# Optimization experiments

Measured on AMD Instinct MI355X. Metric: run time of the kernel, lower is better.

Reference implementation:

```python
import jax, jax.numpy as jnp
import numpy as np

WIN = (7, 7)
SHIFT = (3, 3)
HEADS = 12


def _rel_index():
    wh, ww = WIN
    coords = np.stack(np.meshgrid(np.arange(wh), np.arange(ww), indexing='ij')).reshape(2, -1)
    rel = (coords[:, :, None] - coords[:, None, :]).transpose(1, 2, 0).astype(np.int64)
    rel[:, :, 0] += wh - 1
    rel[:, :, 1] += ww - 1
    rel[:, :, 0] *= 2 * ww - 1
    return rel.sum(-1).reshape(-1)  # [N*N]


def _attn_mask(pH, pW, sh, sw):
    wh, ww = WIN
    mask = np.zeros((pH, pW), np.float32)
    h_sl = [(0, pH - wh), (pH - wh, pH - sh), (pH - sh, pH)]
    w_sl = [(0, pW - ww), (pW - ww, pW - sw), (pW - sw, pW)]
    cnt = 0
    for hs in h_sl:
        for ws in w_sl:
            mask[hs[0]:hs[1], ws[0]:ws[1]] = cnt
            cnt += 1
    nw = (pH // wh) * (pW // ww)
    mask = mask.reshape(pH // wh, wh, pW // ww, ww).transpose(0, 2, 1, 3).reshape(nw, wh * ww)
    diff = mask[:, None, :] - mask[:, :, None]
    return jnp.asarray(np.where(diff != 0, -100.0, 0.0).astype(np.float32))  # [nw, N, N]


def setup_inputs() -> dict:
    key = jax.random.key(0)
    ks = jax.random.split(key, 6)
    C = 384
    return {
        'x': jax.random.normal(ks[0], (16, 56, 56, C), jnp.float32),
        'qkv_weight': jax.random.normal(ks[1], (3 * C, C), jnp.float32) * 0.02,
        'qkv_bias': jax.random.normal(ks[2], (3 * C,), jnp.float32) * 0.02,
        'proj_weight': jax.random.normal(ks[3], (C, C), jnp.float32) * 0.02,
        'proj_bias': jax.random.normal(ks[4], (C,), jnp.float32) * 0.02,
        'rel_table': jax.random.normal(ks[5], (169, HEADS), jnp.float32) * 0.02,
    }


def reference(x, qkv_weight, qkv_bias, proj_weight, proj_bias, rel_table):
    B, H, W, C = x.shape
    wh, ww = WIN
    pad_b = (wh - H % wh) % wh
    pad_r = (ww - W % ww) % ww
    xp = jnp.pad(x, ((0, 0), (0, pad_b), (0, pad_r), (0, 0)))
    pH, pW = H + pad_b, W + pad_r
    sh = 0 if wh >= pH else SHIFT[0]
    sw = 0 if ww >= pW else SHIFT[1]
    shifted = (sh + sw) > 0
    if shifted:
        xp = jnp.roll(xp, (-sh, -sw), axis=(1, 2))
    nwh, nww = pH // wh, pW // ww
    nw, N = nwh * nww, wh * ww
    # window partition -> [B*nw, N, C]
    xw = xp.reshape(B, nwh, wh, nww, ww, C).transpose(0, 1, 3, 2, 4, 5).reshape(B * nw, N, C)
    qkv = xw @ qkv_weight.T + qkv_bias
    qkv = qkv.reshape(B * nw, N, 3, HEADS, C // HEADS).transpose(2, 0, 3, 1, 4)
    q, k, v = qkv[0], qkv[1], qkv[2]  # [B*nw, heads, N, hd]
    q = q * (C // HEADS) ** -0.5
    attn = jnp.einsum('whnd,whmd->whnm', q, k)
    bias = rel_table[jnp.asarray(_rel_index())].reshape(N, N, HEADS).transpose(2, 0, 1)
    attn = attn + bias[None]
    if shifted:
        mask = _attn_mask(pH, pW, sh, sw)  # [nw, N, N]
        attn = (attn.reshape(B, nw, HEADS, N, N) + mask[None, :, None]).reshape(B * nw, HEADS, N, N)
    attn = jax.nn.softmax(attn, axis=-1)
    out = jnp.einsum('whnm,whmd->whnd', attn, v).transpose(0, 2, 1, 3).reshape(B * nw, N, C)
    out = out @ proj_weight.T + proj_bias
    out = out.reshape(B, nwh, nww, wh, ww, C).transpose(0, 1, 3, 2, 4, 5).reshape(B, pH, pW, C)
    if shifted:
        out = jnp.roll(out, (sh, sw), axis=(1, 2))
    return out[:, :H, :W, :]
```

## Files before the change

kernel.cpp:

```cpp
#include <hip/hip_runtime.h>

#define CCH 384
#define NHEADS 12
#define HDIM 32
#define NTOK 49
#define NWIN 1024
#define MROWS 50176
#define PSTR 72

typedef __attribute__((ext_vector_type(8))) short bf16x8;
typedef __attribute__((ext_vector_type(4))) float f32x4;

#define WAITVM_BAR(N) asm volatile("s_waitcnt vmcnt(" #N ")\n\ts_barrier" ::: "memory")
#define BAR() asm volatile("s_barrier" ::: "memory")

__device__ __forceinline__ unsigned short f2bf(float f) {
    unsigned u = __builtin_bit_cast(unsigned, f);
    u += 0x7FFFu + ((u >> 16) & 1u);
    return (unsigned short)(u >> 16);
}

__device__ __forceinline__ void g2lds16(const unsigned short* g, unsigned short* l) {
    __builtin_amdgcn_global_load_lds(
        (const __attribute__((address_space(1))) unsigned int*)g,
        (__attribute__((address_space(3))) unsigned int*)l,
        16, 0, 0);
}

__global__ void prep_kernel(const float* __restrict__ qkvw, const float* __restrict__ projw,
                            const float* __restrict__ rel_table,
                            unsigned short* __restrict__ wq, unsigned short* __restrict__ wp,
                            float* __restrict__ btt2) {
    int i = blockIdx.x * 256 + threadIdx.x;
    if (i < 3 * CCH * CCH) wq[i] = f2bf(qkvw[i]);
    if (i < CCH * CCH) wp[i] = f2bf(projw[i]);
    if (i < 4 * NHEADS * 16 * 64) {
        int cls = i / (NHEADS * 16 * 64);
        int rem = i - cls * (NHEADS * 16 * 64);
        int h = rem / (16 * 64);
        int rem2 = rem - h * (16 * 64);
        int rb = rem2 >> 6, cj = rem2 & 63;
        int jreg = 0;
        if (cj < NTOK) {
            int jy = cj / 7, jx = cj - jy * 7;
            int ry = (cls & 2) ? ((jy < 4) ? 1 : 2) : 0;
            int rx = (cls & 1) ? ((jx < 4) ? 1 : 2) : 0;
            jreg = ry * 3 + rx;
        }
        float4 o;
        float* po = (float*)&o;
#pragma unroll
        for (int rr = 0; rr < 4; ++rr) {
            int ri = rb * 4 + rr;
            float v = -1e30f;
            if (ri < NTOK && cj < NTOK) {
                int iy = ri / 7, ix = ri - iy * 7;
                int jy = cj / 7, jx = cj - jy * 7;
                int idx = (iy - jy + 6) * 13 + (ix - jx + 6);
                v = rel_table[idx * NHEADS + h];
                int ry = (cls & 2) ? ((iy < 4) ? 1 : 2) : 0;
                int rx = (cls & 1) ? ((ix < 4) ? 1 : 2) : 0;
                if (ry * 3 + rx != jreg) v -= 100.f;
            }
            po[rr] = v;
        }
        *(float4*)&btt2[(size_t)i * 4] = o;
    }
}

__device__ __forceinline__ size_t row_to_pixel(int r) {
    int wlin = r / 49, n = r - wlin * 49;
    int b = wlin >> 6, wimg = wlin & 63;
    int wy = wimg >> 3, wx = wimg & 7;
    int iy = n / 7, ix = n - iy * 7;
    int y = wy * 7 + iy + 3; if (y >= 56) y -= 56;
    int x = wx * 7 + ix + 3; if (x >= 56) x -= 56;
    return (size_t)((b * 56 + y) * 56 + x);
}

__global__ __launch_bounds__(256) void gather_kernel(const float* __restrict__ xin,
                                                     unsigned short* __restrict__ xw) {
    int idx = blockIdx.x * 256 + threadIdx.x;
    int row = idx / 96, c4 = (idx - row * 96) * 4;
    const float4 v = *(const float4*)(xin + row_to_pixel(row) * CCH + c4);
    ushort4 o;
    o.x = f2bf(v.x); o.y = f2bf(v.y); o.z = f2bf(v.z); o.w = f2bf(v.w);
    *(ushort4*)(xw + (size_t)row * CCH + c4) = o;
}

__global__ __launch_bounds__(512) void qkv_gemm(const unsigned short* __restrict__ xw,
        const unsigned short* __restrict__ wq, const float* __restrict__ qkv_bias,
        unsigned short* __restrict__ qb, unsigned short* __restrict__ kb,
        unsigned short* __restrict__ vb) {
    __shared__ unsigned short As[2][256 * 32];
    __shared__ unsigned short Bs[2][128 * 32];
    const int tid = threadIdx.x;
    const int bid = blockIdx.x;
    const int xcd = bid & 7;
    const int base = (xcd < 4) ? xcd * 221 : (4 * 221 + (xcd - 4) * 220);
    const int swz = base + (bid >> 3);
    const int rb = swz / 9, cb = swz - rb * 9;
    const int row0 = rb * 256;
    const int col0 = cb * 128;
    const int lane = tid & 63, wv = tid >> 6;
    const int wm = wv >> 1, wn = wv & 1;
    const int l15 = lane & 15, g = lane >> 4;

    const int lrow = lane >> 2;
    const int lc = lane & 3;
    const int scs = ((lc ^ ((lrow >> 1) & 3)) * 8);
    const unsigned short* gA0 = xw + (size_t)(row0 + wv * 32 + lrow) * CCH + scs;
    const unsigned short* gA1 = gA0 + (size_t)16 * CCH;
    const unsigned short* gB0 = wq + (size_t)(col0 + wv * 16 + lrow) * CCH + scs;
    const int rc = (g ^ ((l15 >> 1) & 3)) * 8;

    f32x4 acc[4][4];
#pragma unroll
    for (int i = 0; i < 4; ++i)
#pragma unroll
        for (int j = 0; j < 4; ++j) acc[i][j] = (f32x4){0.f, 0.f, 0.f, 0.f};

    g2lds16(gA0, &As[0][wv * 1024]);
    g2lds16(gA1, &As[0][wv * 1024 + 512]);
    g2lds16(gB0, &Bs[0][wv * 512]);

#pragma unroll
    for (int kk = 0; kk < 12; ++kk) {
        const int cur = kk & 1;
        if (kk < 11) {
            const int nxt = cur ^ 1;
            g2lds16(gA0 + (kk + 1) * 32, &As[nxt][wv * 1024]);
            g2lds16(gA1 + (kk + 1) * 32, &As[nxt][wv * 1024 + 512]);
            g2lds16(gB0 + (kk + 1) * 32, &Bs[nxt][wv * 512]);
            WAITVM_BAR(3);
        } else {
            WAITVM_BAR(0);
        }
        bf16x8 af[4], bfv[4];
#pragma unroll
        for (int mt = 0; mt < 4; ++mt)
            af[mt] = *(const bf16x8*)&As[cur][(wm * 64 + mt * 16 + l15) * 32 + rc];
#pragma unroll
        for (int nt = 0; nt < 4; ++nt)
            bfv[nt] = *(const bf16x8*)&Bs[cur][(wn * 64 + nt * 16 + l15) * 32 + rc];
#pragma unroll
        for (int mt = 0; mt < 4; ++mt)
#pragma unroll
            for (int nt = 0; nt < 4; ++nt)
                acc[mt][nt] = __builtin_amdgcn_mfma_f32_16x16x32_bf16(af[mt], bfv[nt], acc[mt][nt], 0, 0, 0);
        BAR();
    }

    const float SCALE = 0.17677669529663687f;
#pragma unroll
    for (int nt = 0; nt < 4; ++nt) {
        int col = col0 + wn * 64 + nt * 16 + l15;
        float bias = qkv_bias[col];
        int which = col / CCH;
        int rem = col - which * CCH;
        int h = rem >> 5, d = rem & 31;
        unsigned short* dstb = (which == 0) ? qb : ((which == 1) ? kb : vb);
        float scl = (which == 0) ? SCALE : 1.0f;
#pragma unroll
        for (int mt = 0; mt < 4; ++mt) {
#pragma unroll
            for (int rr = 0; rr < 4; ++rr) {
                int row = row0 + wm * 64 + mt * 16 + g * 4 + rr;
                int w2 = row / 49, n2 = row - w2 * 49;
                size_t inst = (size_t)(w2 * NHEADS + h);
                float v = (acc[mt][nt][rr] + bias) * scl;
                dstb[(inst * NTOK + n2) * HDIM + d] = f2bf(v);
            }
        }
    }
}

__global__ __launch_bounds__(256) void attn_kernel(const unsigned short* __restrict__ qbuf,
        const unsigned short* __restrict__ kbuf, const unsigned short* __restrict__ vbuf,
        const float* __restrict__ btt2, unsigned short* __restrict__ ao) {
    __shared__ unsigned short Ps[4][64 * PSTR];
    __shared__ unsigned short Vt[4][32 * 64];
    const int tid = threadIdx.x;
    const int lane = tid & 63, wv = tid >> 6;
    const int inst = blockIdx.x * 4 + wv;
    const int w = inst / NHEADS, h = inst - w * NHEADS;
    const int l15 = lane & 15, g = lane >> 4;
    const unsigned short* qp = qbuf + (size_t)inst * (NTOK * HDIM);
    const unsigned short* kp = kbuf + (size_t)inst * (NTOK * HDIM);
    const unsigned short* vp = vbuf + (size_t)inst * (NTOK * HDIM);

    const bf16x8 zero8 = {0, 0, 0, 0, 0, 0, 0, 0};
    bf16x8 vpre[4];
#pragma unroll
    for (int p = 0; p < 4; ++p) {
        int e0 = (p * 64 + lane) * 8;
        int tok = e0 >> 5;
        vpre[p] = (tok < NTOK) ? *(const bf16x8*)&vp[e0] : zero8;
    }

    bf16x8 aq[4], bk[4];
#pragma unroll
    for (int mt = 0; mt < 4; ++mt) {
        int row = mt * 16 + l15;
        aq[mt] = (row < NTOK) ? *(const bf16x8*)&qp[row * HDIM + g * 8] : zero8;
    }
#pragma unroll
    for (int nt = 0; nt < 4; ++nt) {
        int colk = nt * 16 + l15;
        bk[nt] = (colk < NTOK) ? *(const bf16x8*)&kp[colk * HDIM + g * 8] : zero8;
    }
    f32x4 s[4][4];
#pragma unroll
    for (int mt = 0; mt < 4; ++mt)
#pragma unroll
        for (int nt = 0; nt < 4; ++nt)
            s[mt][nt] = __builtin_amdgcn_mfma_f32_16x16x32_bf16(aq[mt], bk[nt], (f32x4){0.f, 0.f, 0.f, 0.f}, 0, 0, 0);

    {
        unsigned short* vt = Vt[wv];
#pragma unroll
        for (int p = 0; p < 4; ++p) {
            int e0 = (p * 64 + lane) * 8;
            int tok = e0 >> 5, d0 = e0 & 31;
#pragma unroll
            for (int j = 0; j < 8; ++j) {
                int d = d0 + j;
                vt[d * 64 + (tok ^ ((d & 7) << 3))] = (unsigned short)vpre[p][j];
            }
        }
    }

    const int wimg = w & 63;
    const int wy = wimg >> 3, wx = wimg & 7;
    const int wcls = (((wy == 7) ? 2 : 0) | ((wx == 7) ? 1 : 0));
    const float4* bt4 = (const float4*)btt2 + ((size_t)(wcls * NHEADS + h)) * (16 * 64);

    float inv[4][4];
#pragma unroll
    for (int mt = 0; mt < 4; ++mt) {
        float4 bias4[4];
#pragma unroll
        for (int nt = 0; nt < 4; ++nt)
            bias4[nt] = bt4[(mt * 4 + g) * 64 + nt * 16 + l15];
#pragma unroll
        for (int rr = 0; rr < 4; ++rr) {
#pragma unroll
            for (int nt = 0; nt < 4; ++nt) {
                float bb = (rr == 0) ? bias4[nt].x : (rr == 1) ? bias4[nt].y : (rr == 2) ? bias4[nt].z : bias4[nt].w;
                s[mt][nt][rr] += bb;
            }
            float m = fmaxf(fmaxf(s[mt][0][rr], s[mt][1][rr]), fmaxf(s[mt][2][rr], s[mt][3][rr]));
            m = fmaxf(m, __shfl_xor(m, 1));
            m = fmaxf(m, __shfl_xor(m, 2));
            m = fmaxf(m, __shfl_xor(m, 4));
            m = fmaxf(m, __shfl_xor(m, 8));
            float sum = 0.f;
#pragma unroll
            for (int nt = 0; nt < 4; ++nt) {
                float p = __expf(s[mt][nt][rr] - m);
                s[mt][nt][rr] = p;
                sum += p;
            }
            sum += __shfl_xor(sum, 1);
            sum += __shfl_xor(sum, 2);
            sum += __shfl_xor(sum, 4);
            sum += __shfl_xor(sum, 8);
            inv[mt][rr] = 1.0f / sum;
        }
    }
    unsigned short* ps = Ps[wv];
#pragma unroll
    for (int mt = 0; mt < 4; ++mt)
#pragma unroll
        for (int nt = 0; nt < 4; ++nt)
#pragma unroll
            for (int rr = 0; rr < 4; ++rr)
                ps[(mt * 16 + g * 4 + rr) * PSTR + nt * 16 + l15] = f2bf(s[mt][nt][rr]);

    f32x4 o[4][2];
#pragma unroll
    for (int mt = 0; mt < 4; ++mt)
#pragma unroll
        for (int dt = 0; dt < 2; ++dt) o[mt][dt] = (f32x4){0.f, 0.f, 0.f, 0.f};

    const unsigned short* vt = Vt[wv];
#pragma unroll
    for (int kt = 0; kt < 2; ++kt) {
        bf16x8 ap[4];
#pragma unroll
        for (int mt = 0; mt < 4; ++mt)
            ap[mt] = *(const bf16x8*)&ps[(mt * 16 + l15) * PSTR + kt * 32 + g * 8];
#pragma unroll
        for (int dt = 0; dt < 2; ++dt) {
            const int d = dt * 16 + l15;
            const int cb = kt * 32 + g * 8;
            bf16x8 bv = *(const bf16x8*)&vt[d * 64 + (cb ^ ((d & 7) << 3))];
#pragma unroll
            for (int mt = 0; mt < 4; ++mt)
                o[mt][dt] = __builtin_amdgcn_mfma_f32_16x16x32_bf16(ap[mt], bv, o[mt][dt], 0, 0, 0);
        }
    }
#pragma unroll
    for (int mt = 0; mt < 4; ++mt)
#pragma unroll
        for (int dt = 0; dt < 2; ++dt)
#pragma unroll
            for (int rr = 0; rr < 4; ++rr) {
                int row = mt * 16 + g * 4 + rr;
                if (row < NTOK) {
                    float val = o[mt][dt][rr] * inv[mt][rr];
                    ao[((size_t)(w * NTOK + row)) * CCH + h * HDIM + dt * 16 + l15] = f2bf(val);
                }
            }
}

__global__ __launch_bounds__(256) void proj_gemm(const unsigned short* __restrict__ ain,
        const unsigned short* __restrict__ wp, const float* __restrict__ proj_bias,
        float* __restrict__ out) {
    __shared__ unsigned short As[2][128 * 32];
    __shared__ unsigned short Bs[2][128 * 32];
    const int tid = threadIdx.x;
    const int row0 = blockIdx.x * 128;
    const int col0 = blockIdx.y * 128;
    const int lane = tid & 63, wv = tid >> 6;
    const int wm = wv >> 1, wn = wv & 1;
    const int l15 = lane & 15, g = lane >> 4;

    const int srow = wv * 16 + (lane >> 2);
    const int scs = (((lane & 3) ^ ((srow >> 1) & 3)) * 8);
    const unsigned short* gA0 = ain + (size_t)(row0 + srow) * CCH + scs;
    const unsigned short* gA1 = gA0 + (size_t)64 * CCH;
    const unsigned short* gB0 = wp + (size_t)(col0 + srow) * CCH + scs;
    const unsigned short* gB1 = gB0 + (size_t)64 * CCH;
    const int rc = (g ^ ((l15 >> 1) & 3)) * 8;

    f32x4 acc[4][4];
#pragma unroll
    for (int i = 0; i < 4; ++i)
#pragma unroll
        for (int j = 0; j < 4; ++j) acc[i][j] = (f32x4){0.f, 0.f, 0.f, 0.f};

    g2lds16(gA0, &As[0][wv * 512]);
    g2lds16(gA1, &As[0][wv * 512 + 2048]);
    g2lds16(gB0, &Bs[0][wv * 512]);
    g2lds16(gB1, &Bs[0][wv * 512 + 2048]);

#pragma unroll
    for (int kk = 0; kk < 12; ++kk) {
        const int cur = kk & 1;
        if (kk < 11) {
            const int nxt = cur ^ 1;
            g2lds16(gA0 + (kk + 1) * 32, &As[nxt][wv * 512]);
            g2lds16(gA1 + (kk + 1) * 32, &As[nxt][wv * 512 + 2048]);
            g2lds16(gB0 + (kk + 1) * 32, &Bs[nxt][wv * 512]);
            g2lds16(gB1 + (kk + 1) * 32, &Bs[nxt][wv * 512 + 2048]);
            WAITVM_BAR(4);
        } else {
            WAITVM_BAR(0);
        }
        bf16x8 af[4], bfv[4];
#pragma unroll
        for (int mt = 0; mt < 4; ++mt)
            af[mt] = *(const bf16x8*)&As[cur][(wm * 64 + mt * 16 + l15) * 32 + rc];
#pragma unroll
        for (int nt = 0; nt < 4; ++nt)
            bfv[nt] = *(const bf16x8*)&Bs[cur][(wn * 64 + nt * 16 + l15) * 32 + rc];
#pragma unroll
        for (int mt = 0; mt < 4; ++mt)
#pragma unroll
            for (int nt = 0; nt < 4; ++nt)
                acc[mt][nt] = __builtin_amdgcn_mfma_f32_16x16x32_bf16(af[mt], bfv[nt], acc[mt][nt], 0, 0, 0);
        BAR();
    }
#pragma unroll
    for (int nt = 0; nt < 4; ++nt) {
        int col = col0 + wn * 64 + nt * 16 + l15;
        float bias = proj_bias[col];
#pragma unroll
        for (int mt = 0; mt < 4; ++mt) {
#pragma unroll
            for (int rr = 0; rr < 4; ++rr) {
                int row = row0 + wm * 64 + mt * 16 + g * 4 + rr;
                out[row_to_pixel(row) * CCH + col] = acc[mt][nt][rr] + bias;
            }
        }
    }
}

extern "C" void kernel_launch(void* const* d_in, const int* in_sizes, int n_in,
                              void* d_out, int out_size, void* d_ws, size_t ws_size,
                              hipStream_t stream) {
    const float* x     = (const float*)d_in[0];
    const float* qkvw  = (const float*)d_in[1];
    const float* qkvb  = (const float*)d_in[2];
    const float* projw = (const float*)d_in[3];
    const float* projb = (const float*)d_in[4];
    const float* rel   = (const float*)d_in[5];
    float* out = (float*)d_out;

    char* ws = (char*)d_ws;
    unsigned short* wqb = (unsigned short*)(ws);
    unsigned short* wpb = (unsigned short*)(ws + 884736);
    float* btt2         = (float*)(ws + 884736 + 294912);
    const size_t off  = 2097152;
    const size_t bufb = 38535168ull;
    unsigned short* qb  = (unsigned short*)(ws + off);
    unsigned short* kb  = (unsigned short*)(ws + off + bufb);
    unsigned short* vb  = (unsigned short*)(ws + off + 2 * bufb);
    unsigned short* ao  = (unsigned short*)(ws + off + 3 * bufb);
    unsigned short* xw  = ao;

    prep_kernel<<<1728, 256, 0, stream>>>(qkvw, projw, rel, wqb, wpb, btt2);
    gather_kernel<<<18816, 256, 0, stream>>>(x, xw);
    qkv_gemm<<<1764, 512, 0, stream>>>(xw, wqb, qkvb, qb, kb, vb);
    attn_kernel<<<3072, 256, 0, stream>>>(qb, kb, vb, btt2, ao);
    proj_gemm<<<dim3(392, 3), 256, 0, stream>>>(ao, wpb, projb, out);
}
```

Baseline: 173.4 us.

## Deepen QKV GEMM K-tile to 64 with interleaved staged loads and MFMA priority

The QKV GEMM now uses a K-tile of 64 instead of 32, which halves the number of outer iterations. It also changes the LDS swizzle to an 8-way XOR layout. Each iteration is split into four MFMA phases separated by barriers, and the global-to-LDS prefetch loads for the next tile are spread across those phases. s_setprio raises wave priority around the MFMA bursts. The aim is better overlap of loads with matrix math and fewer loop overhead/barrier costs per K. The cost is double the LDS footprint, which may reduce occupancy, and more barriers per iteration.

```diff
diff --git a/kernel.cpp b/kernel.cpp
--- a/kernel.cpp
+++ b/kernel.cpp
@@ -92,27 +92,30 @@
         const unsigned short* __restrict__ wq, const float* __restrict__ qkv_bias,
         unsigned short* __restrict__ qb, unsigned short* __restrict__ kb,
         unsigned short* __restrict__ vb) {
-    __shared__ unsigned short As[2][256 * 32];
-    __shared__ unsigned short Bs[2][128 * 32];
+    __shared__ unsigned short As[2][256 * 64];
+    __shared__ unsigned short Bs[2][128 * 64];
     const int tid = threadIdx.x;
     const int bid = blockIdx.x;
     const int xcd = bid & 7;
     const int base = (xcd < 4) ? xcd * 221 : (4 * 221 + (xcd - 4) * 220);
     const int swz = base + (bid >> 3);
-    const int rb = swz / 9, cb = swz - rb * 9;
-    const int row0 = rb * 256;
-    const int col0 = cb * 128;
+    const int rbk = swz / 9, cbk = swz - rbk * 9;
+    const int row0 = rbk * 256;
+    const int col0 = cbk * 128;
     const int lane = tid & 63, wv = tid >> 6;
     const int wm = wv >> 1, wn = wv & 1;
     const int l15 = lane & 15, g = lane >> 4;
 
-    const int lrow = lane >> 2;
-    const int lc = lane & 3;
-    const int scs = ((lc ^ ((lrow >> 1) & 3)) * 8);
-    const unsigned short* gA0 = xw + (size_t)(row0 + wv * 32 + lrow) * CCH + scs;
-    const unsigned short* gA1 = gA0 + (size_t)16 * CCH;
-    const unsigned short* gB0 = wq + (size_t)(col0 + wv * 16 + lrow) * CCH + scs;
-    const int rc = (g ^ ((l15 >> 1) & 3)) * 8;
+    const int lr8 = lane >> 3;
+    const int lc8 = lane & 7;
+    const unsigned short* gA = xw + (size_t)(row0 + wv * 32 + lr8) * CCH + ((lc8 ^ lr8) * 8);
+    const unsigned short* gB = wq + (size_t)(col0 + wv * 16 + lr8) * CCH + ((lc8 ^ lr8) * 8);
+
+    const int aro = (wm * 64 + l15) * 64;
+    const int bro = (wn * 64 + l15) * 64;
+    const int cf = g ^ (l15 & 7);
+    const int c0s = cf * 8;
+    const int c1s = (cf ^ 4) * 8;
 
     f32x4 acc[4][4];
 #pragma unroll
@@ -120,34 +123,101 @@
 #pragma unroll
         for (int j = 0; j < 4; ++j) acc[i][j] = (f32x4){0.f, 0.f, 0.f, 0.f};
 
-    g2lds16(gA0, &As[0][wv * 1024]);
-    g2lds16(gA1, &As[0][wv * 1024 + 512]);
-    g2lds16(gB0, &Bs[0][wv * 512]);
-
-#pragma unroll
-    for (int kk = 0; kk < 12; ++kk) {
-        const int cur = kk & 1;
-        if (kk < 11) {
-            const int nxt = cur ^ 1;
-            g2lds16(gA0 + (kk + 1) * 32, &As[nxt][wv * 1024]);
-            g2lds16(gA1 + (kk + 1) * 32, &As[nxt][wv * 1024 + 512]);
-            g2lds16(gB0 + (kk + 1) * 32, &Bs[nxt][wv * 512]);
-            WAITVM_BAR(3);
+    g2lds16(gA,            &As[0][(wv * 32 + 0) * 64]);
+    g2lds16(gA + 3072,     &As[0][(wv * 32 + 8) * 64]);
+    g2lds16(gA + 2 * 3072, &As[0][(wv * 32 + 16) * 64]);
+    g2lds16(gA + 3 * 3072, &As[0][(wv * 32 + 24) * 64]);
+    g2lds16(gB,            &Bs[0][(wv * 16 + 0) * 64]);
+    g2lds16(gB + 3072,     &Bs[0][(wv * 16 + 8) * 64]);
+    WAITVM_BAR(0);
+
+#pragma unroll
+    for (int t = 0; t < 6; ++t) {
+        const int bcur = t & 1;
+        const unsigned short* Ab = &As[bcur][0];
+        const unsigned short* Bb = &Bs[bcur][0];
+        unsigned short* An = &As[bcur ^ 1][0];
+        unsigned short* Bn = &Bs[bcur ^ 1][0];
+        const int tn = t + 1;
+        bf16x8 af0, af1, af2, af3, bv0, bv1;
+
+        if (t < 5) {
+            g2lds16(gA + tn * 64,        An + (wv * 32 + 0) * 64);
+            g2lds16(gA + tn * 64 + 3072, An + (wv * 32 + 8) * 64);
+            WAITVM_BAR(2);
         } else {
             WAITVM_BAR(0);
         }
-        bf16x8 af[4], bfv[4];
-#pragma unroll
-        for (int mt = 0; mt < 4; ++mt)
-            af[mt] = *(const bf16x8*)&As[cur][(wm * 64 + mt * 16 + l15) * 32 + rc];
-#pragma unroll
-        for (int nt = 0; nt < 4; ++nt)
-            bfv[nt] = *(const bf16x8*)&Bs[cur][(wn * 64 + nt * 16 + l15) * 32 + rc];
-#pragma unroll
-        for (int mt = 0; mt < 4; ++mt)
-#pragma unroll
-            for (int nt = 0; nt < 4; ++nt)
-                acc[mt][nt] = __builtin_amdgcn_mfma_f32_16x16x32_bf16(af[mt], bfv[nt], acc[mt][nt], 0, 0, 0);
+        af0 = *(const bf16x8*)&Ab[aro + 0 * 1024 + c0s];
+        af1 = *(const bf16x8*)&Ab[aro + 1 * 1024 + c0s];
+        af2 = *(const bf16x8*)&Ab[aro + 2 * 1024 + c0s];
+        af3 = *(const bf16x8*)&Ab[aro + 3 * 1024 + c0s];
+        bv0 = *(const bf16x8*)&Bb[bro + 0 * 1024 + c0s];
+        bv1 = *(const bf16x8*)&Bb[bro + 1 * 1024 + c0s];
+        __builtin_amdgcn_s_setprio(1);
+        acc[0][0] = __builtin_amdgcn_mfma_f32_16x16x32_bf16(af0, bv0, acc[0][0], 0, 0, 0);
+        acc[1][0] = __builtin_amdgcn_mfma_f32_16x16x32_bf16(af1, bv0, acc[1][0], 0, 0, 0);
+        acc[2][0] = __builtin_amdgcn_mfma_f32_16x16x32_bf16(af2, bv0, acc[2][0], 0, 0, 0);
+        acc[3][0] = __builtin_amdgcn_mfma_f32_16x16x32_bf16(af3, bv0, acc[3][0], 0, 0, 0);
+        acc[0][1] = __builtin_amdgcn_mfma_f32_16x16x32_bf16(af0, bv1, acc[0][1], 0, 0, 0);
+        acc[1][1] = __builtin_amdgcn_mfma_f32_16x16x32_bf16(af1, bv1, acc[1][1], 0, 0, 0);
+        acc[2][1] = __builtin_amdgcn_mfma_f32_16x16x32_bf16(af2, bv1, acc[2][1], 0, 0, 0);
+        acc[3][1] = __builtin_amdgcn_mfma_f32_16x16x32_bf16(af3, bv1, acc[3][1], 0, 0, 0);
+        __builtin_amdgcn_s_setprio(0);
+        BAR();
+
+        if (t < 5) {
+            g2lds16(gA + tn * 64 + 2 * 3072, An + (wv * 32 + 16) * 64);
+            g2lds16(gA + tn * 64 + 3 * 3072, An + (wv * 32 + 24) * 64);
+        }
+        bv0 = *(const bf16x8*)&Bb[bro + 2 * 1024 + c0s];
+        bv1 = *(const bf16x8*)&Bb[bro + 3 * 1024 + c0s];
+        __builtin_amdgcn_s_setprio(1);
+        acc[0][2] = __builtin_amdgcn_mfma_f32_16x16x32_bf16(af0, bv0, acc[0][2], 0, 0, 0);
+        acc[1][2] = __builtin_amdgcn_mfma_f32_16x16x32_bf16(af1, bv0, acc[1][2], 0, 0, 0);
+        acc[2][2] = __builtin_amdgcn_mfma_f32_16x16x32_bf16(af2, bv0, acc[2][2], 0, 0, 0);
+        acc[3][2] = __builtin_amdgcn_mfma_f32_16x16x32_bf16(af3, bv0, acc[3][2], 0, 0, 0);
+        acc[0][3] = __builtin_amdgcn_mfma_f32_16x16x32_bf16(af0, bv1, acc[0][3], 0, 0, 0);
+        acc[1][3] = __builtin_amdgcn_mfma_f32_16x16x32_bf16(af1, bv1, acc[1][3], 0, 0, 0);
+        acc[2][3] = __builtin_amdgcn_mfma_f32_16x16x32_bf16(af2, bv1, acc[2][3], 0, 0, 0);
+        acc[3][3] = __builtin_amdgcn_mfma_f32_16x16x32_bf16(af3, bv1, acc[3][3], 0, 0, 0);
+        __builtin_amdgcn_s_setprio(0);
+        BAR();
+
+        if (t < 5) {
+            g2lds16(gB + tn * 64,        Bn + (wv * 16 + 0) * 64);
+            g2lds16(gB + tn * 64 + 3072, Bn + (wv * 16 + 8) * 64);
+        }
+        af0 = *(const bf16x8*)&Ab[aro + 0 * 1024 + c1s];
+        af1 = *(const bf16x8*)&Ab[aro + 1 * 1024 + c1s];
+        af2 = *(const bf16x8*)&Ab[aro + 2 * 1024 + c1s];
+        af3 = *(const bf16x8*)&Ab[aro + 3 * 1024 + c1s];
+        bv0 = *(const bf16x8*)&Bb[bro + 0 * 1024 + c1s];
+        bv1 = *(const bf16x8*)&Bb[bro + 1 * 1024 + c1s];
+        __builtin_amdgcn_s_setprio(1);
+        acc[0][0] = __builtin_amdgcn_mfma_f32_16x16x32_bf16(af0, bv0, acc[0][0], 0, 0, 0);
+        acc[1][0] = __builtin_amdgcn_mfma_f32_16x16x32_bf16(af1, bv0, acc[1][0], 0, 0, 0);
+        acc[2][0] = __builtin_amdgcn_mfma_f32_16x16x32_bf16(af2, bv0, acc[2][0], 0, 0, 0);
+        acc[3][0] = __builtin_amdgcn_mfma_f32_16x16x32_bf16(af3, bv0, acc[3][0], 0, 0, 0);
+        acc[0][1] = __builtin_amdgcn_mfma_f32_16x16x32_bf16(af0, bv1, acc[0][1], 0, 0, 0);
+        acc[1][1] = __builtin_amdgcn_mfma_f32_16x16x32_bf16(af1, bv1, acc[1][1], 0, 0, 0);
+        acc[2][1] = __builtin_amdgcn_mfma_f32_16x16x32_bf16(af2, bv1, acc[2][1], 0, 0, 0);
+        acc[3][1] = __builtin_amdgcn_mfma_f32_16x16x32_bf16(af3, bv1, acc[3][1], 0, 0, 0);
+        __builtin_amdgcn_s_setprio(0);
+        BAR();
+
+        bv0 = *(const bf16x8*)&Bb[bro + 2 * 1024 + c1s];
+        bv1 = *(const bf16x8*)&Bb[bro + 3 * 1024 + c1s];
+        __builtin_amdgcn_s_setprio(1);
+        acc[0][2] = __builtin_amdgcn_mfma_f32_16x16x32_bf16(af0, bv0, acc[0][2], 0, 0, 0);
+        acc[1][2] = __builtin_amdgcn_mfma_f32_16x16x32_bf16(af1, bv0, acc[1][2], 0, 0, 0);
+        acc[2][2] = __builtin_amdgcn_mfma_f32_16x16x32_bf16(af2, bv0, acc[2][2], 0, 0, 0);
+        acc[3][2] = __builtin_amdgcn_mfma_f32_16x16x32_bf16(af3, bv0, acc[3][2], 0, 0, 0);
+        acc[0][3] = __builtin_amdgcn_mfma_f32_16x16x32_bf16(af0, bv1, acc[0][3], 0, 0, 0);
+        acc[1][3] = __builtin_amdgcn_mfma_f32_16x16x32_bf16(af1, bv1, acc[1][3], 0, 0, 0);
+        acc[2][3] = __builtin_amdgcn_mfma_f32_16x16x32_bf16(af2, bv1, acc[2][3], 0, 0, 0);
+        acc[3][3] = __builtin_amdgcn_mfma_f32_16x16x32_bf16(af3, bv1, acc[3][3], 0, 0, 0);
+        __builtin_amdgcn_s_setprio(0);
         BAR();
     }
 
```

Result: slower. 189.5 us (+9.3%).

## Merge prep and gather kernels; shrink QKV GEMM tile to 128x128

Applied to the files above, without the earlier changes.

The weight/bias preparation kernel and the window gather kernel become one launch, with the block index choosing which job a block does. This removes a kernel launch and the serial gap between the two. The QKV GEMM tile drops from 256x128 with 512 threads to 128x128 with 256 threads, and each wave now issues two A loads and two B loads per k-step. That doubles the grid and uses a simpler XCD swizzle, trading less reuse per tile for more blocks and likely higher occupancy.

```diff
diff --git a/kernel.cpp b/kernel.cpp
--- a/kernel.cpp
+++ b/kernel.cpp
@@ -27,11 +27,33 @@
         16, 0, 0);
 }
 
-__global__ void prep_kernel(const float* __restrict__ qkvw, const float* __restrict__ projw,
+__device__ __forceinline__ size_t row_to_pixel(int r) {
+    int wlin = r / 49, n = r - wlin * 49;
+    int b = wlin >> 6, wimg = wlin & 63;
+    int wy = wimg >> 3, wx = wimg & 7;
+    int iy = n / 7, ix = n - iy * 7;
+    int y = wy * 7 + iy + 3; if (y >= 56) y -= 56;
+    int x = wx * 7 + ix + 3; if (x >= 56) x -= 56;
+    return (size_t)((b * 56 + y) * 56 + x);
+}
+
+__global__ __launch_bounds__(256) void prep_gather(const float* __restrict__ xin,
+                            unsigned short* __restrict__ xw,
+                            const float* __restrict__ qkvw, const float* __restrict__ projw,
                             const float* __restrict__ rel_table,
                             unsigned short* __restrict__ wq, unsigned short* __restrict__ wp,
                             float* __restrict__ btt2) {
-    int i = blockIdx.x * 256 + threadIdx.x;
+    const int blk = blockIdx.x;
+    if (blk < 18816) {
+        int idx = blk * 256 + threadIdx.x;
+        int row = idx / 96, c4 = (idx - row * 96) * 4;
+        const float4 v = *(const float4*)(xin + row_to_pixel(row) * CCH + c4);
+        ushort4 o;
+        o.x = f2bf(v.x); o.y = f2bf(v.y); o.z = f2bf(v.z); o.w = f2bf(v.w);
+        *(ushort4*)(xw + (size_t)row * CCH + c4) = o;
+        return;
+    }
+    int i = (blk - 18816) * 256 + threadIdx.x;
     if (i < 3 * CCH * CCH) wq[i] = f2bf(qkvw[i]);
     if (i < CCH * CCH) wp[i] = f2bf(projw[i]);
     if (i < 4 * NHEADS * 16 * 64) {
@@ -68,50 +90,28 @@
     }
 }
 
-__device__ __forceinline__ size_t row_to_pixel(int r) {
-    int wlin = r / 49, n = r - wlin * 49;
-    int b = wlin >> 6, wimg = wlin & 63;
-    int wy = wimg >> 3, wx = wimg & 7;
-    int iy = n / 7, ix = n - iy * 7;
-    int y = wy * 7 + iy + 3; if (y >= 56) y -= 56;
-    int x = wx * 7 + ix + 3; if (x >= 56) x -= 56;
-    return (size_t)((b * 56 + y) * 56 + x);
-}
-
-__global__ __launch_bounds__(256) void gather_kernel(const float* __restrict__ xin,
-                                                     unsigned short* __restrict__ xw) {
-    int idx = blockIdx.x * 256 + threadIdx.x;
-    int row = idx / 96, c4 = (idx - row * 96) * 4;
-    const float4 v = *(const float4*)(xin + row_to_pixel(row) * CCH + c4);
-    ushort4 o;
-    o.x = f2bf(v.x); o.y = f2bf(v.y); o.z = f2bf(v.z); o.w = f2bf(v.w);
-    *(ushort4*)(xw + (size_t)row * CCH + c4) = o;
-}
-
-__global__ __launch_bounds__(512) void qkv_gemm(const unsigned short* __restrict__ xw,
+__global__ __launch_bounds__(256) void qkv_gemm(const unsigned short* __restrict__ xw,
         const unsigned short* __restrict__ wq, const float* __restrict__ qkv_bias,
         unsigned short* __restrict__ qb, unsigned short* __restrict__ kb,
         unsigned short* __restrict__ vb) {
-    __shared__ unsigned short As[2][256 * 32];
+    __shared__ unsigned short As[2][128 * 32];
     __shared__ unsigned short Bs[2][128 * 32];
     const int tid = threadIdx.x;
     const int bid = blockIdx.x;
-    const int xcd = bid & 7;
-    const int base = (xcd < 4) ? xcd * 221 : (4 * 221 + (xcd - 4) * 220);
-    const int swz = base + (bid >> 3);
+    const int swz = (bid & 7) * 441 + (bid >> 3);
     const int rb = swz / 9, cb = swz - rb * 9;
-    const int row0 = rb * 256;
+    const int row0 = rb * 128;
     const int col0 = cb * 128;
     const int lane = tid & 63, wv = tid >> 6;
     const int wm = wv >> 1, wn = wv & 1;
     const int l15 = lane & 15, g = lane >> 4;
 
-    const int lrow = lane >> 2;
-    const int lc = lane & 3;
-    const int scs = ((lc ^ ((lrow >> 1) & 3)) * 8);
-    const unsigned short* gA0 = xw + (size_t)(row0 + wv * 32 + lrow) * CCH + scs;
-    const unsigned short* gA1 = gA0 + (size_t)16 * CCH;
-    const unsigned short* gB0 = wq + (size_t)(col0 + wv * 16 + lrow) * CCH + scs;
+    const int srow = wv * 16 + (lane >> 2);
+    const int scs = (((lane & 3) ^ ((srow >> 1) & 3)) * 8);
+    const unsigned short* gA0 = xw + (size_t)(row0 + srow) * CCH + scs;
+    const unsigned short* gA1 = gA0 + (size_t)64 * CCH;
+    const unsigned short* gB0 = wq + (size_t)(col0 + srow) * CCH + scs;
+    const unsigned short* gB1 = gB0 + (size_t)64 * CCH;
     const int rc = (g ^ ((l15 >> 1) & 3)) * 8;
 
     f32x4 acc[4][4];
@@ -120,19 +120,21 @@
 #pragma unroll
         for (int j = 0; j < 4; ++j) acc[i][j] = (f32x4){0.f, 0.f, 0.f, 0.f};
 
-    g2lds16(gA0, &As[0][wv * 1024]);
-    g2lds16(gA1, &As[0][wv * 1024 + 512]);
+    g2lds16(gA0, &As[0][wv * 512]);
+    g2lds16(gA1, &As[0][wv * 512 + 2048]);
     g2lds16(gB0, &Bs[0][wv * 512]);
+    g2lds16(gB1, &Bs[0][wv * 512 + 2048]);
 
 #pragma unroll
     for (int kk = 0; kk < 12; ++kk) {
         const int cur = kk & 1;
         if (kk < 11) {
             const int nxt = cur ^ 1;
-            g2lds16(gA0 + (kk + 1) * 32, &As[nxt][wv * 1024]);
-            g2lds16(gA1 + (kk + 1) * 32, &As[nxt][wv * 1024 + 512]);
+            g2lds16(gA0 + (kk + 1) * 32, &As[nxt][wv * 512]);
+            g2lds16(gA1 + (kk + 1) * 32, &As[nxt][wv * 512 + 2048]);
             g2lds16(gB0 + (kk + 1) * 32, &Bs[nxt][wv * 512]);
-            WAITVM_BAR(3);
+            g2lds16(gB1 + (kk + 1) * 32, &Bs[nxt][wv * 512 + 2048]);
+            WAITVM_BAR(4);
         } else {
             WAITVM_BAR(0);
         }
@@ -410,9 +412,8 @@
     unsigned short* ao  = (unsigned short*)(ws + off + 3 * bufb);
     unsigned short* xw  = ao;
 
-    prep_kernel<<<1728, 256, 0, stream>>>(qkvw, projw, rel, wqb, wpb, btt2);
-    gather_kernel<<<18816, 256, 0, stream>>>(x, xw);
-    qkv_gemm<<<1764, 512, 0, stream>>>(xw, wqb, qkvb, qb, kb, vb);
+    prep_gather<<<20544, 256, 0, stream>>>(x, xw, qkvw, projw, rel, wqb, wpb, btt2);
+    qkv_gemm<<<3528, 256, 0, stream>>>(xw, wqb, qkvb, qb, kb, vb);
     attn_kernel<<<3072, 256, 0, stream>>>(qb, kb, vb, btt2, ao);
     proj_gemm<<<dim3(392, 3), 256, 0, stream>>>(ao, wpb, projb, out);
 }
```

After: 175.6 us. Within noise of the previous version (+1.3%).
